# Performance work log

Hardware: AMD Instinct MI355X
Metric: run time of the kernel (lower is better)

Reference implementation:

```python
import jax, jax.numpy as jnp
import numpy as np

B, DIM_X, K = 16384, 2048, 128


def setup_inputs() -> dict:
    key = jax.random.key(0)
    k_x, k_y, k_z, k_ew, k_eb, k_dw = jax.random.split(key, 6)
    x = jax.random.normal(k_x, (B, DIM_X), dtype=jnp.float32)
    # targets are +/-1 (sign labels, matching sign(y_hat)==y accuracy check)
    y = jnp.sign(jax.random.normal(k_y, (B,), dtype=jnp.float32))
    y = jnp.where(y == 0, 1.0, y)
    z = jax.random.randint(k_z, (B,), 0, K)
    # torch.nn.Linear default init: U(-1/sqrt(fan_in), 1/sqrt(fan_in))
    be = 1.0 / np.sqrt(DIM_X)
    enc_W = jax.random.uniform(k_ew, (K, DIM_X), jnp.float32, -be, be)
    enc_b = jax.random.uniform(k_eb, (K,), jnp.float32, -be, be)
    # torch.nn.Bilinear weight shape [out=1, in1=K, in2=DIM_X], U(-1/sqrt(in1), 1/sqrt(in1))
    bd = 1.0 / np.sqrt(K)
    dec_W = jax.random.uniform(k_dw, (1, K, DIM_X), jnp.float32, -bd, bd)
    dec_bias = jnp.zeros((K,), dtype=jnp.float32)
    return {"x": x, "y": y, "z": z, "enc_W": enc_W, "enc_b": enc_b,
            "dec_W": dec_W, "dec_bias": dec_bias}


def reference(x, y, z, enc_W, enc_b, dec_W, dec_bias):
    # encoder: single Linear (num_layers=1)
    s = x @ enc_W.T + enc_b                      # [B, K]
    # argmax_onehot: hard one-hot routing (eval mode, no gumbel)
    z_hat_index = jnp.argmax(s, axis=-1)          # [B]
    z_tilde = jax.nn.one_hot(z_hat_index, s.shape[-1], dtype=s.dtype)  # [B, K]
    # Bilinear(K, dim_X, 1, bias=False) + z_tilde @ decoder_bias
    y_hat = jnp.einsum('bk,kd,bd->b', z_tilde, dec_W[0], x) + z_tilde @ dec_bias
    loss = jnp.mean(jnp.square(y_hat - y))
    accuracy = jnp.mean((jnp.sign(y_hat) == y).astype(jnp.float32))
    return (y_hat, z_hat_index, loss, accuracy)
```

## Files before the change

kernel.cpp:

```cpp
#include <hip/hip_runtime.h>

#define BB 16384
#define DD 2048
#define KK 128
#define NT 64
#define NCHK 16
#define RPB 64
#define NBLK 256
#define DELTA 8e-3f
#define BUFB 32768
#define FCAP 2048

typedef __attribute__((ext_vector_type(8))) short  bf16x8;
typedef __attribute__((ext_vector_type(4))) float  f32x4;
typedef __attribute__((ext_vector_type(4))) unsigned int u32x4;

union V16 { u32x4 u; f32x4 f; bf16x8 s; };

__device__ __forceinline__ void wg_barrier() {
  asm volatile("s_waitcnt lgkmcnt(0)\n\ts_barrier" ::: "memory");
}

__global__ __launch_bounds__(256) void prep_kernel(
    const float* __restrict__ encW, const float* __restrict__ decW,
    unsigned short* __restrict__ wEh, unsigned short* __restrict__ wDh,
    float* __restrict__ out, unsigned int* __restrict__ counter)
{
  __shared__ float sw[16][260];
  const int bid = blockIdx.x;
  const int tid = threadIdx.x;
  if (bid == 0 && tid == 0) { *counter = 0u; out[2*BB] = 0.f; out[2*BB+1] = 0.f; }
  const int sel = bid >> 6, rem = bid & 63;
  const int ct = rem >> 3, kt = rem & 7;
  const float* W = sel ? decW : encW;
  unsigned short* oh = sel ? wDh : wEh;

  {
    const int row = tid >> 4, seg = tid & 15;
    const float* src = W + (size_t)(ct * 16 + row) * DD + kt * 256 + seg * 16;
#pragma unroll
    for (int i = 0; i < 4; ++i)
      *(f32x4*)&sw[row][seg * 16 + i * 4] = *(const f32x4*)(src + i * 4);
  }
  __syncthreads();

  const int l = tid & 63, wv = tid >> 6;
#pragma unroll
  for (int h = 0; h < 2; ++h) {
    const int tt = wv * 2 + h;
    const int t  = kt * 8 + tt;
    const float* sp = &sw[l & 15][tt * 32 + ((l >> 4) << 3)];
    V16 vh;
#pragma unroll
    for (int p = 0; p < 4; ++p) {
      unsigned hu[2];
#pragma unroll
      for (int q = 0; q < 2; ++q) {
        unsigned u  = __float_as_uint(sp[p * 2 + q]);
        unsigned rh = u + 0x7FFFu + ((u >> 16) & 1u);
        hu[q] = (rh >> 16) & 0xFFFFu;
      }
      vh.u[p] = (hu[1] << 16) | hu[0];
    }
    *(u32x4*)(oh + ((size_t)(t * 8 + ct) * 64 + l) * 8) = vh.u;
  }
}

__global__ __launch_bounds__(1024)
void main_kernel(
    const float* __restrict__ x, const float* __restrict__ y,
    const float* __restrict__ encb, const float* __restrict__ decb,
    const unsigned short* __restrict__ wEh, const unsigned short* __restrict__ wDh,
    float* __restrict__ out, unsigned int* __restrict__ counter,
    float* __restrict__ list)
{
  __shared__ __align__(16) unsigned char pool[86016];
  const int tid = threadIdx.x;
  const int w = tid >> 6, l = tid & 63;
  const int wr = w & 3, wcg = w >> 2;
  const int rbase = blockIdx.x * RPB;

  const int srow = tid >> 4, seg = tid & 15;
  const float* gXc = x + (size_t)(rbase + srow) * DD + seg * 8;
  const int woff = srow * 256 + ((seg ^ (srow & 15)) << 4);

  const unsigned short* gE = wEh + (size_t)(wcg * 1024 + l * 8);
  const unsigned short* gD = wDh + (size_t)(wcg * 1024 + l * 8);

  const int rowb = (wr * 16 + (l & 15)) * 256;
  int blkb[4];
#pragma unroll
  for (int tt = 0; tt < 4; ++tt)
    blkb[tt] = ((tt * 4 + (l >> 4)) ^ (l & 15)) << 4;

  f32x4 accE[2], accD[2];
  const f32x4 zero4 = {0.f, 0.f, 0.f, 0.f};
#pragma unroll
  for (int c = 0; c < 2; ++c) { accE[c] = zero4; accD[c] = zero4; }

  auto WRX = [&](int nb, f32x4 A, f32x4 Bv) {
    float fa[8] = {A[0],A[1],A[2],A[3],Bv[0],Bv[1],Bv[2],Bv[3]};
    V16 vh, vl;
#pragma unroll
    for (int p = 0; p < 4; ++p) {
      unsigned u0 = __float_as_uint(fa[2*p]);
      unsigned u1 = __float_as_uint(fa[2*p+1]);
      vh.u[p] = (u0 >> 16) | (u1 & 0xFFFF0000u);
      float r0 = fa[2*p]   - __uint_as_float(u0 & 0xFFFF0000u);
      float r1 = fa[2*p+1] - __uint_as_float(u1 & 0xFFFF0000u);
      vl.u[p] = (__float_as_uint(r0) >> 16) | (__float_as_uint(r1) & 0xFFFF0000u);
    }
    unsigned char* bp = pool + nb + woff;
    *(u32x4*)bp            = vh.u;
    *(u32x4*)(bp + 16384)  = vl.u;
  };

#define LDB(base, t, off) (*(const bf16x8*)((base) + (size_t)(t) * 4096 + (off)))
#define LDBH(h, e0, e1, d0, d1, f0, f1, g0, g1) do {                 \
    int _t = (h) * 2;                                                \
    e0 = LDB(gE, _t, 0);     e1 = LDB(gE, _t, 512);                  \
    d0 = LDB(gD, _t, 0);     d1 = LDB(gD, _t, 512);                  \
    f0 = LDB(gE, _t + 1, 0); f1 = LDB(gE, _t + 1, 512);              \
    g0 = LDB(gD, _t + 1, 0); g1 = LDB(gD, _t + 1, 512);              \
  } while (0)

#define MFMA(a, b, c) __builtin_amdgcn_mfma_f32_16x16x32_bf16(a, b, c, 0, 0, 0)
#define KSTEP(cbase, tt, E0, E1, D0, D1) do {                                    \
    const unsigned char* ap = pool + (cbase) + rowb + blkb[tt];                  \
    bf16x8 ah = *(const bf16x8*)ap;                                              \
    bf16x8 al = *(const bf16x8*)(ap + 16384);                                    \
    accE[0] = MFMA(ah, E0, accE[0]);                                             \
    accE[1] = MFMA(ah, E1, accE[1]);                                             \
    accD[0] = MFMA(ah, D0, accD[0]);                                             \
    accD[1] = MFMA(ah, D1, accD[1]);                                             \
    accE[0] = MFMA(al, E0, accE[0]);                                             \
    accE[1] = MFMA(al, E1, accE[1]);                                             \
  } while (0)

  bf16x8 Se0,Se1,Sd0,Sd1, Sf0,Sf1,Sg0,Sg1;
  bf16x8 Te0,Te1,Td0,Td1, Tf0,Tf1,Tg0,Tg1;
  f32x4 xA, xB;

  xA = *(const f32x4*)gXc; xB = *(const f32x4*)(gXc + 4);
  LDBH(0, Se0,Se1,Sd0,Sd1, Sf0,Sf1,Sg0,Sg1);
  WRX(0, xA, xB);
  wg_barrier();

  for (int c = 0; c < NCHK; ++c) {
    const int cb = (c & 1) * BUFB;
    const int nb = cb ^ BUFB;
    LDBH(2 * c + 1, Te0,Te1,Td0,Td1, Tf0,Tf1,Tg0,Tg1);
    if (c + 1 < NCHK) {
      const float* p = gXc + (size_t)(c + 1) * 128;
      xA = *(const f32x4*)p; xB = *(const f32x4*)(p + 4);
    }
    __builtin_amdgcn_s_setprio(1);
    KSTEP(cb, 0, Se0, Se1, Sd0, Sd1);
    KSTEP(cb, 1, Sf0, Sf1, Sg0, Sg1);
    __builtin_amdgcn_s_setprio(0);
    if (c + 1 < NCHK)
      LDBH(2 * c + 2, Se0,Se1,Sd0,Sd1, Sf0,Sf1,Sg0,Sg1);
    __builtin_amdgcn_s_setprio(1);
    KSTEP(cb, 2, Te0, Te1, Td0, Td1);
    KSTEP(cb, 3, Tf0, Tf1, Tg0, Tg1);
    __builtin_amdgcn_s_setprio(0);
    if (c + 1 < NCHK) WRX(nb, xA, xB);
    wg_barrier();
  }
#undef LDBH
#undef KSTEP
#undef LDB
#undef MFMA

  float* sT  = (float*)pool;
  float* sS  = (float*)(pool + 33792);
  float* sm1 = (float*)(pool + 66560);
  float* sm2 = (float*)(pool + 67584);
  int*   si1 = (int*)  (pool + 68608);

  {
    const int q = l >> 4, cc = l & 15;
    const int col0 = wcg * 32 + cc;
    const int col1 = col0 + 16;
#pragma unroll
    for (int c = 0; c < 2; ++c) {
      const int col = wcg * 32 + c * 16 + cc;
#pragma unroll
      for (int i = 0; i < 4; ++i)
        sT[(wr * 16 + q * 4 + i) * 132 + col] = accD[c][i];
    }
    const float b0 = encb[col0], b1 = encb[col1];
    float m1v[4], m2v[4]; int i1v[4];
#pragma unroll
    for (int i = 0; i < 4; ++i) {
      const int row = wr * 16 + q * 4 + i;
      float v0 = accE[0][i] + b0;
      float v1 = accE[1][i] + b1;
      sS[row * 128 + col0] = v0;
      sS[row * 128 + col1] = v1;
      if (v0 >= v1) { m1v[i] = v0; m2v[i] = v1; i1v[i] = col0; }
      else          { m1v[i] = v1; m2v[i] = v0; i1v[i] = col1; }
    }
#pragma unroll
    for (int d = 1; d < 16; d <<= 1) {
#pragma unroll
      for (int i = 0; i < 4; ++i) {
        float om1 = __shfl_xor(m1v[i], d);
        float om2 = __shfl_xor(m2v[i], d);
        int   oi  = __shfl_xor(i1v[i], d);
        if (om1 > m1v[i] || (om1 == m1v[i] && oi < i1v[i])) {
          m2v[i] = fmaxf(m1v[i], om2); m1v[i] = om1; i1v[i] = oi;
        } else {
          m2v[i] = fmaxf(m2v[i], om1);
        }
      }
    }
    if (cc == 0) {
#pragma unroll
      for (int i = 0; i < 4; ++i) {
        const int row = wr * 16 + q * 4 + i;
        sm1[row * 4 + wcg] = m1v[i];
        sm2[row * 4 + wcg] = m2v[i];
        si1[row * 4 + wcg] = i1v[i];
      }
    }
  }
  __syncthreads();

  float lossAcc = 0.f, accAcc = 0.f;
  if (tid < RPB) {
    const int row = tid, R = rbase + row;
    float m1 = -3.4e38f, m2 = -3.4e38f; int i1 = 0;
#pragma unroll
    for (int g = 0; g < 4; ++g) {
      float a1 = sm1[row * 4 + g], a2 = sm2[row * 4 + g];
      int ai = si1[row * 4 + g];
      if (a1 > m1) { m2 = fmaxf(m1, a2); m1 = a1; i1 = ai; }
      else         { m2 = fmaxf(m2, a1); }
    }
    float yh = sT[row * 132 + i1] + decb[i1];
    out[R]      = yh;
    out[BB + R] = (float)i1;
    if (m1 - m2 < DELTA) {
      unsigned p = atomicAdd(counter, 1u);
      if (p < (unsigned)FCAP) {
        float* ent = list + (size_t)p * 132;
        ((unsigned*)ent)[0] = (unsigned)R;
        const f32x4* sr = (const f32x4*)(sS + row * 128);
        f32x4* dst = (f32x4*)(ent + 4);
#pragma unroll
        for (int j = 0; j < 32; ++j) dst[j] = sr[j];
      }
    }
    float yv = y[R];
    float d  = yh - yv;
    lossAcc = d * d;
    float sg = (yh > 0.f) ? 1.f : ((yh < 0.f) ? -1.f : 0.f);
    accAcc = (sg == yv) ? 1.f : 0.f;
  }
#pragma unroll
  for (int d = 1; d < 64; d <<= 1) {
    lossAcc += __shfl_xor(lossAcc, d);
    accAcc  += __shfl_xor(accAcc, d);
  }
  if (tid == 0) {
    atomicAdd(&out[2*BB],     lossAcc * (1.f / BB));
    atomicAdd(&out[2*BB + 1], accAcc  * (1.f / BB));
  }
}

__global__ __launch_bounds__(64) void fixup_kernel(
    const float* __restrict__ x, const float* __restrict__ y,
    const float* __restrict__ encW, const float* __restrict__ encb,
    const float* __restrict__ decW, const float* __restrict__ decb,
    float* __restrict__ out,
    const unsigned int* __restrict__ counter, const float* __restrict__ list)
{
  int n = (int)*counter;
  if (n > FCAP) n = FCAP;
  const int l = threadIdx.x;
  for (int e = blockIdx.x; e < n; e += gridDim.x) {
    const float* ent = list + (size_t)e * 132;
    const int R = (int)((const unsigned*)ent)[0];
    const float s0 = ent[4 + 2 * l], s1 = ent[5 + 2 * l];
    float m = fmaxf(s0, s1);
#pragma unroll
    for (int d = 1; d < 64; d <<= 1) m = fmaxf(m, __shfl_xor(m, d));
    const float win = m - 2.0f * DELTA;
    unsigned long long mm0 = __ballot(s0 >= win);
    unsigned long long mm1 = __ballot(s1 >= win);
    const float* xr = x + (size_t)R * DD;
    double best = -1e300; int bk = KK;
    while (mm0 | mm1) {
      int c;
      if (mm0) { int b = __builtin_ctzll(mm0); mm0 &= mm0 - 1; c = 2 * b; }
      else     { int b = __builtin_ctzll(mm1); mm1 &= mm1 - 1; c = 2 * b + 1; }
      const float* wp = encW + (size_t)c * DD;
      double s = 0.0;
#pragma unroll
      for (int j = 0; j < 8; ++j) {
        f32x4 wv = *(const f32x4*)(wp + j * 256 + l * 4);
        f32x4 xv = *(const f32x4*)(xr + j * 256 + l * 4);
        s = fma((double)xv[0], (double)wv[0], s);
        s = fma((double)xv[1], (double)wv[1], s);
        s = fma((double)xv[2], (double)wv[2], s);
        s = fma((double)xv[3], (double)wv[3], s);
      }
#pragma unroll
      for (int d = 1; d < 64; d <<= 1) s += __shfl_xor(s, d);
      s += (double)encb[c];
      if (s > best || (s == best && c < bk)) { best = s; bk = c; }
    }
    const float* dr = decW + (size_t)bk * DD;
    double t = 0.0;
#pragma unroll
    for (int j = 0; j < 8; ++j) {
      f32x4 wv = *(const f32x4*)(dr + j * 256 + l * 4);
      f32x4 xv = *(const f32x4*)(xr + j * 256 + l * 4);
      t = fma((double)xv[0], (double)wv[0], t);
      t = fma((double)xv[1], (double)wv[1], t);
      t = fma((double)xv[2], (double)wv[2], t);
      t = fma((double)xv[3], (double)wv[3], t);
    }
#pragma unroll
    for (int d = 1; d < 64; d <<= 1) t += __shfl_xor(t, d);
    if (l == 0) {
      float yh = (float)(t + (double)decb[bk]);
      float yv = y[R];
      float old = out[R];
      float dn = yh - yv, dol = old - yv;
      atomicAdd(&out[2*BB], (dn*dn - dol*dol) * (1.f / BB));
      float sgn = (yh  > 0.f) ? 1.f : ((yh  < 0.f) ? -1.f : 0.f);
      float sgo = (old > 0.f) ? 1.f : ((old < 0.f) ? -1.f : 0.f);
      float mn = (sgn == yv) ? 1.f : 0.f;
      float mo = (sgo == yv) ? 1.f : 0.f;
      atomicAdd(&out[2*BB + 1], (mn - mo) * (1.f / BB));
      out[R]      = yh;
      out[BB + R] = (float)bk;
    }
  }
}

extern "C" void kernel_launch(void* const* d_in, const int* in_sizes, int n_in,
                              void* d_out, int out_size, void* d_ws, size_t ws_size,
                              hipStream_t stream)
{
  const float* x    = (const float*)d_in[0];
  const float* y    = (const float*)d_in[1];
  const float* encW = (const float*)d_in[3];
  const float* encb = (const float*)d_in[4];
  const float* decW = (const float*)d_in[5];
  const float* decb = (const float*)d_in[6];
  float* out = (float*)d_out;

  unsigned char* ws = (unsigned char*)d_ws;
  unsigned short* wEh = (unsigned short*)ws;
  unsigned short* wDh = (unsigned short*)(ws + 524288);
  unsigned int* counter = (unsigned int*)(ws + 1048576);
  float* list = (float*)(ws + 1048592);

  prep_kernel<<<128, 256, 0, stream>>>(encW, decW, wEh, wDh, out, counter);
  main_kernel<<<NBLK, 1024, 0, stream>>>(x, y, encb, decb, wEh, wDh,
                                         out, counter, list);
  fixup_kernel<<<512, 64, 0, stream>>>(x, y, encW, encb, decW, decb,
                                       out, counter, list);
}
```

Before: 85.46 us.

## Stage weight tiles into LDS via global_load_lds and use 2x2 MFMA tiles per wave

Instead of each wave loading its bf16 weight fragments straight from global memory into registers, the block DMAs each weight chunk into a double-buffered LDS region with global_load_lds and reads it from LDS. Block size drops from 1024 to 512 threads. Each wave now covers two row tiles, so every weight fragment is reused twice, and the chunk size along D is halved to 32 iterations. The aim is to cut redundant global and L2 weight traffic and free registers, at the cost of more LDS reads, fewer waves per block, and a full vmcnt wait at every barrier.

```diff
diff --git a/kernel.cpp b/kernel.cpp
--- a/kernel.cpp
+++ b/kernel.cpp
@@ -4,11 +4,11 @@
 #define DD 2048
 #define KK 128
 #define NT 64
-#define NCHK 16
+#define NCHK 32
 #define RPB 64
 #define NBLK 256
 #define DELTA 8e-3f
-#define BUFB 32768
+#define BUFS 49152
 #define FCAP 2048
 
 typedef __attribute__((ext_vector_type(8))) short  bf16x8;
@@ -17,8 +17,10 @@
 
 union V16 { u32x4 u; f32x4 f; bf16x8 s; };
 
-__device__ __forceinline__ void wg_barrier() {
-  asm volatile("s_waitcnt lgkmcnt(0)\n\ts_barrier" ::: "memory");
+__device__ __forceinline__ void gld16(const void* g, void* l) {
+  __builtin_amdgcn_global_load_lds(
+      (const __attribute__((address_space(1))) void*)g,
+      (__attribute__((address_space(3))) void*)l, 16, 0, 0);
 }
 
 __global__ __launch_bounds__(256) void prep_kernel(
@@ -66,7 +68,7 @@
   }
 }
 
-__global__ __launch_bounds__(1024)
+__global__ __launch_bounds__(512)
 void main_kernel(
     const float* __restrict__ x, const float* __restrict__ y,
     const float* __restrict__ encb, const float* __restrict__ decb,
@@ -74,29 +76,33 @@
     float* __restrict__ out, unsigned int* __restrict__ counter,
     float* __restrict__ list)
 {
-  __shared__ __align__(16) unsigned char pool[86016];
+  __shared__ __align__(16) unsigned char pool[98304];
   const int tid = threadIdx.x;
   const int w = tid >> 6, l = tid & 63;
-  const int wr = w & 3, wcg = w >> 2;
+  const int wr = w >> 2, wcg = w & 3;
   const int rbase = blockIdx.x * RPB;
 
-  const int srow = tid >> 4, seg = tid & 15;
+  const int srow = tid >> 3, seg = tid & 7;
   const float* gXc = x + (size_t)(rbase + srow) * DD + seg * 8;
-  const int woff = srow * 256 + ((seg ^ (srow & 15)) << 4);
-
-  const unsigned short* gE = wEh + (size_t)(wcg * 1024 + l * 8);
-  const unsigned short* gD = wDh + (size_t)(wcg * 1024 + l * 8);
-
-  const int rowb = (wr * 16 + (l & 15)) * 256;
-  int blkb[4];
-#pragma unroll
-  for (int tt = 0; tt < 4; ++tt)
-    blkb[tt] = ((tt * 4 + (l >> 4)) ^ (l & 15)) << 4;
-
-  f32x4 accE[2], accD[2];
+  const int woff = srow * 128 + ((seg ^ (srow & 7)) << 4);
+
+  int rowb[2];
+#pragma unroll
+  for (int rt = 0; rt < 2; ++rt)
+    rowb[rt] = (wr * 32 + rt * 16 + (l & 15)) * 128;
+  int blkb[2];
+#pragma unroll
+  for (int tt = 0; tt < 2; ++tt)
+    blkb[tt] = ((tt * 4 + (l >> 4)) ^ (l & 7)) << 4;
+
+  const int bfo = wcg * 2048 + (l << 4);
+
+  f32x4 accE[2][2], accD[2][2];
   const f32x4 zero4 = {0.f, 0.f, 0.f, 0.f};
 #pragma unroll
-  for (int c = 0; c < 2; ++c) { accE[c] = zero4; accD[c] = zero4; }
+  for (int rt = 0; rt < 2; ++rt)
+#pragma unroll
+    for (int ct = 0; ct < 2; ++ct) { accE[rt][ct] = zero4; accD[rt][ct] = zero4; }
 
   auto WRX = [&](int nb, f32x4 A, f32x4 Bv) {
     float fa[8] = {A[0],A[1],A[2],A[3],Bv[0],Bv[1],Bv[2],Bv[3]};
@@ -111,65 +117,68 @@
       vl.u[p] = (__float_as_uint(r0) >> 16) | (__float_as_uint(r1) & 0xFFFF0000u);
     }
     unsigned char* bp = pool + nb + woff;
-    *(u32x4*)bp            = vh.u;
-    *(u32x4*)(bp + 16384)  = vl.u;
+    *(u32x4*)bp           = vh.u;
+    *(u32x4*)(bp + 8192)  = vl.u;
   };
 
-#define LDB(base, t, off) (*(const bf16x8*)((base) + (size_t)(t) * 4096 + (off)))
-#define LDBH(h, e0, e1, d0, d1, f0, f1, g0, g1) do {                 \
-    int _t = (h) * 2;                                                \
-    e0 = LDB(gE, _t, 0);     e1 = LDB(gE, _t, 512);                  \
-    d0 = LDB(gD, _t, 0);     d1 = LDB(gD, _t, 512);                  \
-    f0 = LDB(gE, _t + 1, 0); f1 = LDB(gE, _t + 1, 512);              \
-    g0 = LDB(gD, _t + 1, 0); g1 = LDB(gD, _t + 1, 512);              \
+  auto DMAB = [&](int nb, int c) {
+    const unsigned short* eb = wEh + (size_t)(2 * c) * 4096 + tid * 8;
+    const unsigned short* db = wDh + (size_t)(2 * c) * 4096 + tid * 8;
+    gld16(eb,        pool + nb + 16384 + w * 1024);
+    gld16(eb + 4096, pool + nb + 24576 + w * 1024);
+    gld16(db,        pool + nb + 32768 + w * 1024);
+    gld16(db + 4096, pool + nb + 40960 + w * 1024);
+  };
+
+#define MFMA(a, b, c) __builtin_amdgcn_mfma_f32_16x16x32_bf16(a, b, c, 0, 0, 0)
+#define KSTEP(cbase, tt) do {                                                    \
+    const unsigned char* bp = pool + (cbase);                                    \
+    const unsigned char* bb = bp + 16384 + (tt) * 8192 + bfo;                    \
+    bf16x8 E0 = *(const bf16x8*)bb;                                              \
+    bf16x8 E1 = *(const bf16x8*)(bb + 1024);                                     \
+    bf16x8 D0 = *(const bf16x8*)(bb + 16384);                                    \
+    bf16x8 D1 = *(const bf16x8*)(bb + 16384 + 1024);                             \
+    _Pragma("unroll")                                                            \
+    for (int rt = 0; rt < 2; ++rt) {                                             \
+      const unsigned char* ap = bp + rowb[rt] + blkb[tt];                        \
+      bf16x8 ah = *(const bf16x8*)ap;                                            \
+      bf16x8 al = *(const bf16x8*)(ap + 8192);                                   \
+      accE[rt][0] = MFMA(ah, E0, accE[rt][0]);                                   \
+      accE[rt][1] = MFMA(ah, E1, accE[rt][1]);                                   \
+      accD[rt][0] = MFMA(ah, D0, accD[rt][0]);                                   \
+      accD[rt][1] = MFMA(ah, D1, accD[rt][1]);                                   \
+      accE[rt][0] = MFMA(al, E0, accE[rt][0]);                                   \
+      accE[rt][1] = MFMA(al, E1, accE[rt][1]);                                   \
+    }                                                                            \
   } while (0)
 
-#define MFMA(a, b, c) __builtin_amdgcn_mfma_f32_16x16x32_bf16(a, b, c, 0, 0, 0)
-#define KSTEP(cbase, tt, E0, E1, D0, D1) do {                                    \
-    const unsigned char* ap = pool + (cbase) + rowb + blkb[tt];                  \
-    bf16x8 ah = *(const bf16x8*)ap;                                              \
-    bf16x8 al = *(const bf16x8*)(ap + 16384);                                    \
-    accE[0] = MFMA(ah, E0, accE[0]);                                             \
-    accE[1] = MFMA(ah, E1, accE[1]);                                             \
-    accD[0] = MFMA(ah, D0, accD[0]);                                             \
-    accD[1] = MFMA(ah, D1, accD[1]);                                             \
-    accE[0] = MFMA(al, E0, accE[0]);                                             \
-    accE[1] = MFMA(al, E1, accE[1]);                                             \
-  } while (0)
-
-  bf16x8 Se0,Se1,Sd0,Sd1, Sf0,Sf1,Sg0,Sg1;
-  bf16x8 Te0,Te1,Td0,Td1, Tf0,Tf1,Tg0,Tg1;
-  f32x4 xA, xB;
-
-  xA = *(const f32x4*)gXc; xB = *(const f32x4*)(gXc + 4);
-  LDBH(0, Se0,Se1,Sd0,Sd1, Sf0,Sf1,Sg0,Sg1);
-  WRX(0, xA, xB);
-  wg_barrier();
+  {
+    f32x4 xA = *(const f32x4*)gXc;
+    f32x4 xB = *(const f32x4*)(gXc + 4);
+    DMAB(0, 0);
+    WRX(0, xA, xB);
+    asm volatile("s_waitcnt vmcnt(0) lgkmcnt(0)" ::: "memory");
+    __builtin_amdgcn_s_barrier();
+  }
 
   for (int c = 0; c < NCHK; ++c) {
-    const int cb = (c & 1) * BUFB;
-    const int nb = cb ^ BUFB;
-    LDBH(2 * c + 1, Te0,Te1,Td0,Td1, Tf0,Tf1,Tg0,Tg1);
+    const int cb = (c & 1) * BUFS;
+    const int nb = cb ^ BUFS;
+    f32x4 xA, xB;
     if (c + 1 < NCHK) {
-      const float* p = gXc + (size_t)(c + 1) * 128;
+      const float* p = gXc + (size_t)(c + 1) * 64;
       xA = *(const f32x4*)p; xB = *(const f32x4*)(p + 4);
+      DMAB(nb, c + 1);
     }
     __builtin_amdgcn_s_setprio(1);
-    KSTEP(cb, 0, Se0, Se1, Sd0, Sd1);
-    KSTEP(cb, 1, Sf0, Sf1, Sg0, Sg1);
-    __builtin_amdgcn_s_setprio(0);
-    if (c + 1 < NCHK)
-      LDBH(2 * c + 2, Se0,Se1,Sd0,Sd1, Sf0,Sf1,Sg0,Sg1);
-    __builtin_amdgcn_s_setprio(1);
-    KSTEP(cb, 2, Te0, Te1, Td0, Td1);
-    KSTEP(cb, 3, Tf0, Tf1, Tg0, Tg1);
+    KSTEP(cb, 0);
+    KSTEP(cb, 1);
     __builtin_amdgcn_s_setprio(0);
     if (c + 1 < NCHK) WRX(nb, xA, xB);
-    wg_barrier();
-  }
-#undef LDBH
+    asm volatile("s_waitcnt vmcnt(0) lgkmcnt(0)" ::: "memory");
+    __builtin_amdgcn_s_barrier();
+  }
 #undef KSTEP
-#undef LDB
 #undef MFMA
 
   float* sT  = (float*)pool;
@@ -183,46 +192,54 @@
     const int col0 = wcg * 32 + cc;
     const int col1 = col0 + 16;
 #pragma unroll
-    for (int c = 0; c < 2; ++c) {
-      const int col = wcg * 32 + c * 16 + cc;
-#pragma unroll
-      for (int i = 0; i < 4; ++i)
-        sT[(wr * 16 + q * 4 + i) * 132 + col] = accD[c][i];
-    }
+    for (int rt = 0; rt < 2; ++rt)
+#pragma unroll
+      for (int ct = 0; ct < 2; ++ct) {
+        const int col = wcg * 32 + ct * 16 + cc;
+#pragma unroll
+        for (int i = 0; i < 4; ++i)
+          sT[(wr * 32 + rt * 16 + q * 4 + i) * 132 + col] = accD[rt][ct][i];
+      }
     const float b0 = encb[col0], b1 = encb[col1];
-    float m1v[4], m2v[4]; int i1v[4];
-#pragma unroll
-    for (int i = 0; i < 4; ++i) {
-      const int row = wr * 16 + q * 4 + i;
-      float v0 = accE[0][i] + b0;
-      float v1 = accE[1][i] + b1;
-      sS[row * 128 + col0] = v0;
-      sS[row * 128 + col1] = v1;
-      if (v0 >= v1) { m1v[i] = v0; m2v[i] = v1; i1v[i] = col0; }
-      else          { m1v[i] = v1; m2v[i] = v0; i1v[i] = col1; }
-    }
+    float m1v[8], m2v[8]; int i1v[8];
+#pragma unroll
+    for (int rt = 0; rt < 2; ++rt)
+#pragma unroll
+      for (int i = 0; i < 4; ++i) {
+        const int j = rt * 4 + i;
+        const int row = wr * 32 + rt * 16 + q * 4 + i;
+        float v0 = accE[rt][0][i] + b0;
+        float v1 = accE[rt][1][i] + b1;
+        sS[row * 128 + col0] = v0;
+        sS[row * 128 + col1] = v1;
+        if (v0 >= v1) { m1v[j] = v0; m2v[j] = v1; i1v[j] = col0; }
+        else          { m1v[j] = v1; m2v[j] = v0; i1v[j] = col1; }
+      }
 #pragma unroll
     for (int d = 1; d < 16; d <<= 1) {
 #pragma unroll
-      for (int i = 0; i < 4; ++i) {
-        float om1 = __shfl_xor(m1v[i], d);
-        float om2 = __shfl_xor(m2v[i], d);
-        int   oi  = __shfl_xor(i1v[i], d);
-        if (om1 > m1v[i] || (om1 == m1v[i] && oi < i1v[i])) {
-          m2v[i] = fmaxf(m1v[i], om2); m1v[i] = om1; i1v[i] = oi;
+      for (int j = 0; j < 8; ++j) {
+        float om1 = __shfl_xor(m1v[j], d);
+        float om2 = __shfl_xor(m2v[j], d);
+        int   oi  = __shfl_xor(i1v[j], d);
+        if (om1 > m1v[j] || (om1 == m1v[j] && oi < i1v[j])) {
+          m2v[j] = fmaxf(m1v[j], om2); m1v[j] = om1; i1v[j] = oi;
         } else {
-          m2v[i] = fmaxf(m2v[i], om1);
+          m2v[j] = fmaxf(m2v[j], om1);
         }
       }
     }
     if (cc == 0) {
 #pragma unroll
-      for (int i = 0; i < 4; ++i) {
-        const int row = wr * 16 + q * 4 + i;
-        sm1[row * 4 + wcg] = m1v[i];
-        sm2[row * 4 + wcg] = m2v[i];
-        si1[row * 4 + wcg] = i1v[i];
-      }
+      for (int rt = 0; rt < 2; ++rt)
+#pragma unroll
+        for (int i = 0; i < 4; ++i) {
+          const int j = rt * 4 + i;
+          const int row = wr * 32 + rt * 16 + q * 4 + i;
+          sm1[row * 4 + wcg] = m1v[j];
+          sm2[row * 4 + wcg] = m2v[j];
+          si1[row * 4 + wcg] = i1v[j];
+        }
     }
   }
   __syncthreads();
@@ -360,8 +377,8 @@
   float* list = (float*)(ws + 1048592);
 
   prep_kernel<<<128, 256, 0, stream>>>(encW, decW, wEh, wDh, out, counter);
-  main_kernel<<<NBLK, 1024, 0, stream>>>(x, y, encb, decb, wEh, wDh,
-                                         out, counter, list);
+  main_kernel<<<NBLK, 512, 0, stream>>>(x, y, encb, decb, wEh, wDh,
+                                        out, counter, list);
   fixup_kernel<<<512, 64, 0, stream>>>(x, y, encW, encb, decW, decb,
                                        out, counter, list);
 }
```

After: 84.02 us, median of 3. No clear change (-1.7%).
